# Kernel tuning notes

Hardware: AMD Instinct MI355X
Metric: run time of the kernel (lower is better)

## Reference

```python
import jax, jax.numpy as jnp
import numpy as np

R_ACT = 8
GROUPS = 32
EPS = 1e-5


def _group_norm(x, gamma, beta):
    # x: [B, C, T]; GroupNorm over (C//G, T) per group, per sample
    B, C, T = x.shape
    xr = x.reshape(B, GROUPS, C // GROUPS, T)
    mu = xr.mean(axis=(2, 3), keepdims=True)
    var = xr.var(axis=(2, 3), keepdims=True)
    xn = ((xr - mu) * jax.lax.rsqrt(var + EPS)).reshape(B, C, T)
    return xn * gamma[None, :, None] + beta[None, :, None]


def _topk_mean(logits, valid_len):
    # logits: [B, T, C]; valid_len: [B] int32. mean of top-k per class, k = max(1, valid_len // r_act)
    B, T, C = logits.shape
    vals = -jnp.sort(-logits, axis=1)            # descending sort along T
    csum = jnp.cumsum(vals, axis=1)              # [B, T, C]
    k = jnp.maximum(1, valid_len // R_ACT).astype(jnp.int32)  # [B]
    idx = jnp.broadcast_to((k - 1)[:, None, None], (B, 1, C))
    sel = jnp.take_along_axis(csum, idx, axis=1)[:, 0, :]     # [B, C]
    return sel / k[:, None].astype(logits.dtype)


def setup_inputs() -> dict:
    key = jax.random.key(0)
    ks = jax.random.split(key, 12)
    B, Fd, T, O, Timg, D, C = 16, 2048, 2048, 512, 2048, 512, 20
    inp = {
        "input_features": jax.random.normal(ks[0], (B, Fd, T), jnp.float32),
        "masks": jnp.ones((B, 1, T), jnp.float32),
        "text_proto": jax.random.normal(ks[1], (1, C, D), jnp.float32),
        "img_feats": jax.random.normal(ks[2], (B, Timg, D), jnp.float32),
        "img_masks": jnp.ones((B, Timg), jnp.float32),
        # 1x1-conv embedding params (2 layers) + GN affines + cls linear
        "W1": jax.random.normal(ks[3], (O, Fd), jnp.float32) * 0.02,
        "b1": jnp.zeros((O,), jnp.float32),
        "g1": jnp.ones((O,), jnp.float32),
        "beta1": jnp.zeros((O,), jnp.float32),
        "W2": jax.random.normal(ks[4], (O, O), jnp.float32) * 0.02,
        "b2": jnp.zeros((O,), jnp.float32),
        "g2": jnp.ones((O,), jnp.float32),
        "beta2": jnp.zeros((O,), jnp.float32),
        "Wc": jax.random.normal(ks[5], (C, O), jnp.float32) * 0.02,
        "bc": jnp.zeros((C,), jnp.float32),
    }
    return inp


def reference(input_features, masks, text_proto, img_feats, img_masks,
              W1, b1, g1, beta1, W2, b2, g2, beta2, Wc, bc):
    # feature embedding: two (1x1 conv -> GN) blocks, mask applied after each
    x = jnp.einsum('of,bft->bot', W1, input_features) + b1[None, :, None]
    x = _group_norm(x, g1, beta1) * masks
    x = jnp.einsum('oc,bct->bot', W2, x) + b2[None, :, None]
    x = _group_norm(x, g2, beta2) * masks            # [B, O, T]
    fe = x.transpose(0, 2, 1)                        # [B, T, O]
    cls_logits = jax.nn.sigmoid(jnp.einsum('bto,co->btc', fe, Wc) + bc)  # [B, T, C]

    tp = text_proto[0].T                             # [D, C]
    text_logits = jnp.einsum('btd,dc->btc', img_feats, tp)  # [B, Timg, C]

    text_len = jax.lax.stop_gradient(img_masks).sum(-1).astype(jnp.int32)      # [B]
    cls_len = jax.lax.stop_gradient(masks).sum(axis=(-2, -1)).astype(jnp.int32)  # [B]
    text_vid_scores = _topk_mean(text_logits, text_len)  # [B, C]
    cls_vid_scores = _topk_mean(cls_logits, cls_len)     # [B, C]
    # stack both heads: [0] = text (inference output), [1] = cls (training output)
    return jnp.stack([text_vid_scores, cls_vid_scores])
```

## Files before the change

### kernel.cpp

```cpp
#include <hip/hip_runtime.h>

typedef unsigned short u16;
typedef unsigned int u32;
typedef unsigned long long u64;

typedef __attribute__((ext_vector_type(8))) __bf16 bf16x8;
typedef __attribute__((ext_vector_type(4))) float f32x4;

__device__ __forceinline__ u16 f2bf(float f) {
  u32 u = __float_as_uint(f);
  u = (u + 0x7fffu + ((u >> 16) & 1u)) >> 16;
  return (u16)u;
}
__device__ __forceinline__ float bf2f(u16 h) {
  return __uint_as_float(((u32)h) << 16);
}

__device__ __forceinline__ void stage16(const u16* g, u16* lds_wave_base) {
#if __has_builtin(__builtin_amdgcn_global_load_lds)
  __builtin_amdgcn_global_load_lds((__attribute__((address_space(1))) u32*)g,
                                   (__attribute__((address_space(3))) u32*)lds_wave_base,
                                   16, 0, 0);
#else
  u16* l = lds_wave_base + (threadIdx.x & 63) * 8;
  *(uint4*)l = *(const uint4*)g;
#endif
}

__device__ __forceinline__ float wred(float v) {
  v += __shfl_xor(v, 1, 64);
  v += __shfl_xor(v, 2, 64);
  v += __shfl_xor(v, 4, 64);
  v += __shfl_xor(v, 8, 64);
  v += __shfl_xor(v, 16, 64);
  v += __shfl_xor(v, 32, 64);
  return v;
}

__global__ void __launch_bounds__(256) f2bf_kernel(const float* __restrict__ in,
                                                   u16* __restrict__ out, int n4) {
  int i = blockIdx.x * 256 + threadIdx.x;
  if (i >= n4) return;
  float4 v = ((const float4*)in)[i];
  u64 p = (u64)f2bf(v.x) | ((u64)f2bf(v.y) << 16) | ((u64)f2bf(v.z) << 32) |
          ((u64)f2bf(v.w) << 48);
  ((u64*)out)[i] = p;
}

__global__ void __launch_bounds__(256) zinit(float* __restrict__ p, int n) {
  int i = blockIdx.x * 256 + threadIdx.x;
  if (i < n) p[i] = 0.f;
}

__global__ void __launch_bounds__(256) transpose_bf16(const float* __restrict__ src,
                                                      u16* __restrict__ dst,
                                                      long long fStride, long long oStride) {
  __shared__ float tile[64][65];
  int b = blockIdx.z;
  const float* s = src + (size_t)b * fStride;
  u16* d = dst + (size_t)b * oStride;
  int tid = threadIdx.x;
  int t0 = blockIdx.x * 64, f0 = blockIdx.y * 64;
  int r = tid >> 2, cq = (tid & 3) * 16;
#pragma unroll
  for (int q = 0; q < 4; ++q) {
    float4 v = *(const float4*)(s + (size_t)(f0 + r) * 2048 + (t0 + cq + q * 4));
    tile[r][cq + q * 4 + 0] = v.x;
    tile[r][cq + q * 4 + 1] = v.y;
    tile[r][cq + q * 4 + 2] = v.z;
    tile[r][cq + q * 4 + 3] = v.w;
  }
  __syncthreads();
  u32 ow[8];
#pragma unroll
  for (int h = 0; h < 8; ++h) {
    float lo = tile[cq + 2 * h + 0][r];
    float hi = tile[cq + 2 * h + 1][r];
    ow[h] = (u32)f2bf(lo) | ((u32)f2bf(hi) << 16);
  }
  u16* dp = d + (size_t)(t0 + r) * 2048 + f0 + cq;
  uint4 v0 = {ow[0], ow[1], ow[2], ow[3]};
  uint4 v1 = {ow[4], ow[5], ow[6], ow[7]};
  *(uint4*)dp = v0;
  *(uint4*)(dp + 8) = v1;
}

#define BAR() __builtin_amdgcn_s_barrier()
#define LGKM0() asm volatile("s_waitcnt lgkmcnt(0)" ::: "memory")
#define VMC4() asm volatile("s_waitcnt vmcnt(4)" ::: "memory")
#define VMC0() asm volatile("s_waitcnt vmcnt(0)" ::: "memory")

__device__ __forceinline__ void rdA4(const u16 (&sAb)[256][32], int mh, int wm, int ln, int sl,
                                     bf16x8 (&af)[4]) {
#pragma unroll
  for (int mi = 0; mi < 4; ++mi)
    af[mi] = *(const bf16x8*)&sAb[wm * 128 + mh * 64 + mi * 16 + ln][sl];
}
__device__ __forceinline__ void rdB4(const u16 (&sBb)[256][32], int wn, int ln, int sl,
                                     bf16x8 (&bfr)[4]) {
#pragma unroll
  for (int ni = 0; ni < 4; ++ni)
    bfr[ni] = *(const bf16x8*)&sBb[wn * 64 + ni * 16 + ln][sl];
}
__device__ __forceinline__ void mfma8(f32x4 (&acc)[8][4], const bf16x8 (&af)[4],
                                      const bf16x8 (&bfr)[4], int mh) {
  __builtin_amdgcn_s_setprio(1);
#pragma unroll
  for (int mi = 0; mi < 4; ++mi)
#pragma unroll
    for (int ni = 0; ni < 4; ++ni)
      acc[mh * 4 + mi][ni] = __builtin_amdgcn_mfma_f32_16x16x32_bf16(
          af[mi], bfr[ni], acc[mh * 4 + mi][ni], 0, 0, 0);
  __builtin_amdgcn_s_setprio(0);
}
__device__ __forceinline__ void stg2(const u16* g0, const u16* g1, u16 (&dst)[256][32],
                                     int wid, int koff) {
  stage16(g0 + koff, &dst[wid * 32][0]);
  stage16(g1 + koff, &dst[wid * 32 + 16][0]);
}

template <bool MASKED>
__global__ void __launch_bounds__(512, 2) gemm8(const u16* __restrict__ A,
                                                const u16* __restrict__ A0,
                                                const u16* __restrict__ Bw,
                                                size_t bStride,
                                                const float* __restrict__ t1,
                                                const float* __restrict__ t2,
                                                const float* __restrict__ mkp,
                                                float* __restrict__ sOut,
                                                float* __restrict__ ssOut,
                                                u16* __restrict__ Out,
                                                int M, int N, int K) {
  __shared__ u16 sA[2][2][256][32];
  __shared__ u16 sB[2][2][256][32];
  int tid = threadIdx.x;
  int bz = blockIdx.z;
  int m0 = blockIdx.x * 256, n0 = blockIdx.y * 256;
  const u16* Ab = (bz == 0) ? A0 : (A + (size_t)bz * M * K);
  const u16* Bb = Bw + (size_t)bz * bStride;
  int lane = tid & 63, wid = tid >> 6;
  int wm = wid >> 2, wn = wid & 3;
  int ln = lane & 15, lm = lane >> 4;
  int sl = (lm ^ (ln & 3)) * 8;
  int lrow = lane >> 2;
  int swz = (lane & 3) ^ (lrow & 3);
  const u16* gA0 = Ab + (size_t)(m0 + wid * 32 + lrow) * K + swz * 8;
  const u16* gA1 = gA0 + (size_t)16 * K;
  const u16* gB0 = Bb + (size_t)(n0 + wid * 32 + lrow) * K + swz * 8;
  const u16* gB1 = gB0 + (size_t)16 * K;

  f32x4 acc[8][4];
#pragma unroll
  for (int mi = 0; mi < 8; ++mi)
#pragma unroll
    for (int ni = 0; ni < 4; ++ni) acc[mi][ni] = (f32x4){0.f, 0.f, 0.f, 0.f};

  bf16x8 af[4], bfr[4];

  stg2(gA0, gA1, sA[0][0], wid, 0);
  stg2(gB0, gB1, sB[0][0], wid, 0);
  stg2(gA0, gA1, sA[0][1], wid, 32);
  stg2(gB0, gB1, sB[0][1], wid, 32);
  stg2(gA0, gA1, sA[1][0], wid, 64);
  stg2(gB0, gB1, sB[1][0], wid, 64);
  VMC4();
  BAR();

  int NI = K >> 7;
  int kt0 = 0;
  for (int I = 0; I < NI - 1; ++I, kt0 += 2) {
    int kb1 = (kt0 + 1) * 64 + 32;
    int kb2 = (kt0 + 2) * 64;
    int kb3 = (kt0 + 2) * 64 + 32;
    int kb4 = (kt0 + 3) * 64;
    rdB4(sB[0][0], wn, ln, sl, bfr);
    rdA4(sA[0][0], 0, wm, ln, sl, af);
    stg2(gA0, gA1, sA[1][1], wid, kb1);
    BAR(); LGKM0(); mfma8(acc, af, bfr, 0); BAR();
    rdA4(sA[0][0], 1, wm, ln, sl, af);
    stg2(gB0, gB1, sB[1][1], wid, kb1);
    BAR(); LGKM0(); mfma8(acc, af, bfr, 1); BAR();
    rdB4(sB[0][1], wn, ln, sl, bfr);
    rdA4(sA[0][1], 0, wm, ln, sl, af);
    stg2(gA0, gA1, sA[0][0], wid, kb2);
    BAR(); LGKM0(); mfma8(acc, af, bfr, 0); BAR();
    rdA4(sA[0][1], 1, wm, ln, sl, af);
    stg2(gB0, gB1, sB[0][0], wid, kb2);
    BAR(); LGKM0(); mfma8(acc, af, bfr, 1);
    VMC4(); BAR();
    rdB4(sB[1][0], wn, ln, sl, bfr);
    rdA4(sA[1][0], 0, wm, ln, sl, af);
    stg2(gA0, gA1, sA[0][1], wid, kb3);
    BAR(); LGKM0(); mfma8(acc, af, bfr, 0); BAR();
    rdA4(sA[1][0], 1, wm, ln, sl, af);
    stg2(gB0, gB1, sB[0][1], wid, kb3);
    BAR(); LGKM0(); mfma8(acc, af, bfr, 1); BAR();
    rdB4(sB[1][1], wn, ln, sl, bfr);
    rdA4(sA[1][1], 0, wm, ln, sl, af);
    stg2(gA0, gA1, sA[1][0], wid, kb4);
    BAR(); LGKM0(); mfma8(acc, af, bfr, 0); BAR();
    rdA4(sA[1][1], 1, wm, ln, sl, af);
    stg2(gB0, gB1, sB[1][0], wid, kb4);
    BAR(); LGKM0(); mfma8(acc, af, bfr, 1);
    VMC4(); BAR();
  }
  {
    int kb1 = (kt0 + 1) * 64 + 32;
    rdB4(sB[0][0], wn, ln, sl, bfr);
    rdA4(sA[0][0], 0, wm, ln, sl, af);
    stg2(gA0, gA1, sA[1][1], wid, kb1);
    BAR(); LGKM0(); mfma8(acc, af, bfr, 0); BAR();
    rdA4(sA[0][0], 1, wm, ln, sl, af);
    stg2(gB0, gB1, sB[1][1], wid, kb1);
    BAR(); LGKM0(); mfma8(acc, af, bfr, 1); BAR();
    rdB4(sB[0][1], wn, ln, sl, bfr);
    rdA4(sA[0][1], 0, wm, ln, sl, af);
    BAR(); LGKM0(); mfma8(acc, af, bfr, 0); BAR();
    rdA4(sA[0][1], 1, wm, ln, sl, af);
    BAR(); LGKM0(); mfma8(acc, af, bfr, 1);
    VMC0(); BAR();
    rdB4(sB[1][0], wn, ln, sl, bfr);
    rdA4(sA[1][0], 0, wm, ln, sl, af);
    BAR(); LGKM0(); mfma8(acc, af, bfr, 0); BAR();
    rdA4(sA[1][0], 1, wm, ln, sl, af);
    BAR(); LGKM0(); mfma8(acc, af, bfr, 1); BAR();
    rdB4(sB[1][1], wn, ln, sl, bfr);
    rdA4(sA[1][1], 0, wm, ln, sl, af);
    BAR(); LGKM0(); mfma8(acc, af, bfr, 0); BAR();
    rdA4(sA[1][1], 1, wm, ln, sl, af);
    LGKM0(); mfma8(acc, af, bfr, 1);
  }

  const float* t1p = MASKED ? (t1 + (size_t)bz * N) : t1;
  float t1v[4], t2v[4];
#pragma unroll
  for (int ni = 0; ni < 4; ++ni) {
    int ncol = n0 + wn * 64 + ni * 16 + ln;
    t1v[ni] = t1p[ncol];
    t2v[ni] = MASKED ? t2[ncol] : 0.f;
  }
  float sp[4] = {0.f, 0.f, 0.f, 0.f}, ssp[4] = {0.f, 0.f, 0.f, 0.f};
  u16* ob = Out + (size_t)bz * M * N;
#pragma unroll
  for (int mi = 0; mi < 8; ++mi) {
    int mrow = m0 + wm * 128 + mi * 16 + lm * 4;
    float mka[4] = {1.f, 1.f, 1.f, 1.f};
    if constexpr (MASKED) {
      float4 mv = *(const float4*)(mkp + (size_t)bz * M + mrow);
      mka[0] = mv.x; mka[1] = mv.y; mka[2] = mv.z; mka[3] = mv.w;
    }
#pragma unroll
    for (int ni = 0; ni < 4; ++ni) {
      int ncol = n0 + wn * 64 + ni * 16 + ln;
#pragma unroll
      for (int r = 0; r < 4; ++r) {
        float v = acc[mi][ni][r] + t1v[ni];
        if constexpr (MASKED) v = v * mka[r] + t2v[ni];
        sp[ni] += v;
        ssp[ni] += v * v;
        ob[(size_t)(mrow + r) * N + ncol] = f2bf(v);
      }
    }
  }
#pragma unroll
  for (int ni = 0; ni < 4; ++ni) {
    float S = wred(sp[ni]);
    float SS = wred(ssp[ni]);
    if (lane == 0) {
      int grp = blockIdx.y * 16 + wn * 4 + ni;
      atomicAdd(&sOut[bz * 32 + grp], S);
      atomicAdd(&ssOut[bz * 32 + grp], SS);
    }
  }
}

__global__ void __launch_bounds__(512) gnstats(const float* __restrict__ sS,
                                               const float* __restrict__ sSS,
                                               const float* __restrict__ gamma,
                                               const float* __restrict__ beta,
                                               float* __restrict__ gmO,
                                               float* __restrict__ gdO) {
  int b = blockIdx.x;
  int c = threadIdx.x;
  int g = c >> 4;
  const float cnt = 16.f * 2048.f;
  float mu = sS[b * 32 + g] / cnt;
  float var = sSS[b * 32 + g] / cnt - mu * mu;
  float inv = rsqrtf(var + 1e-5f);
  float gm = gamma[c] * inv;
  gmO[(size_t)b * 512 + c] = gm;
  gdO[(size_t)b * 512 + c] = beta[c] - mu * gm;
}

__global__ void __launch_bounds__(256) wfold(const float* __restrict__ W2,
                                             const float* __restrict__ gm1,
                                             const float* __restrict__ bt1,
                                             u16* __restrict__ W2f,
                                             float* __restrict__ beta2) {
  int w = blockIdx.x * 4 + (threadIdx.x >> 6);
  int lane = threadIdx.x & 63;
  int b = w >> 9, o = w & 511;
  const float* wr = W2 + (size_t)o * 512 + lane * 8;
  const float* gmr = gm1 + (size_t)b * 512 + lane * 8;
  const float* btr = bt1 + (size_t)b * 512 + lane * 8;
  float4 w0 = *(const float4*)wr, w1 = *(const float4*)(wr + 4);
  float4 g0 = *(const float4*)gmr, g1v = *(const float4*)(gmr + 4);
  float4 t0 = *(const float4*)btr, t1v = *(const float4*)(btr + 4);
  float wv[8] = {w0.x, w0.y, w0.z, w0.w, w1.x, w1.y, w1.z, w1.w};
  float gv[8] = {g0.x, g0.y, g0.z, g0.w, g1v.x, g1v.y, g1v.z, g1v.w};
  float tv[8] = {t0.x, t0.y, t0.z, t0.w, t1v.x, t1v.y, t1v.z, t1v.w};
  u32 ow[4];
  float acc = 0.f;
#pragma unroll
  for (int h = 0; h < 4; ++h) {
    float lo = wv[2 * h] * gv[2 * h];
    float hi = wv[2 * h + 1] * gv[2 * h + 1];
    ow[h] = (u32)f2bf(lo) | ((u32)f2bf(hi) << 16);
    acc += wv[2 * h] * tv[2 * h] + wv[2 * h + 1] * tv[2 * h + 1];
  }
  uint4 o4 = {ow[0], ow[1], ow[2], ow[3]};
  *(uint4*)(W2f + ((size_t)b * 512 + o) * 512 + lane * 8) = o4;
  acc = wred(acc);
  if (lane == 0) beta2[(size_t)b * 512 + o] = acc;
}

template <typename TX, bool CLS>
__global__ void __launch_bounds__(512) head_v2(const TX* __restrict__ X,
                                               const float* __restrict__ W,
                                               const float* __restrict__ bcv,
                                               const float* __restrict__ gma,
                                               const float* __restrict__ gad,
                                               const float* __restrict__ masks,
                                               float* __restrict__ Out, int Tdim) {
  __shared__ float red[64 * 20];
  int tid = threadIdx.x;
  int tl = tid & 63;
  int ks = __builtin_amdgcn_readfirstlane(tid >> 6);
  int b = blockIdx.y;
  int t = blockIdx.x * 64 + tl;
  for (int i = tid; i < 64 * 20; i += 512) red[i] = 0.f;
  float acc[20];
#pragma unroll
  for (int c = 0; c < 20; ++c) acc[c] = 0.f;
  const TX* xr = X + ((size_t)b * Tdim + t) * 512 + ks * 64;
  const float* Wk = W + ks * 64;
  const float* gmk = CLS ? (gma + (size_t)b * 512 + ks * 64) : nullptr;
  const float* gak = CLS ? (gad + (size_t)b * 512 + ks * 64) : nullptr;
  __syncthreads();
#pragma unroll
  for (int kk = 0; kk < 64; kk += 8) {
    float xv[8];
    if constexpr (sizeof(TX) == 2) {
      uint4 v = *(const uint4*)(xr + kk);
      u32 wv[4] = {v.x, v.y, v.z, v.w};
#pragma unroll
      for (int h = 0; h < 4; ++h) {
        xv[2 * h] = bf2f((u16)(wv[h] & 0xffffu));
        xv[2 * h + 1] = bf2f((u16)(wv[h] >> 16));
      }
    } else {
      float4 p0 = *(const float4*)(xr + kk);
      float4 p1 = *(const float4*)(xr + kk + 4);
      xv[0] = p0.x; xv[1] = p0.y; xv[2] = p0.z; xv[3] = p0.w;
      xv[4] = p1.x; xv[5] = p1.y; xv[6] = p1.z; xv[7] = p1.w;
    }
    if constexpr (CLS) {
#pragma unroll
      for (int j = 0; j < 8; ++j) xv[j] = xv[j] * gmk[kk + j] + gak[kk + j];
    }
#pragma unroll
    for (int c = 0; c < 20; ++c) {
      const float* wr = &Wk[c * 512 + kk];
#pragma unroll
      for (int j = 0; j < 8; ++j) acc[c] += xv[j] * wr[j];
    }
  }
#pragma unroll
  for (int c = 0; c < 20; ++c) atomicAdd(&red[tl * 20 + c], acc[c]);
  __syncthreads();
  if (tid < 64) {
    float mk = CLS ? masks[(size_t)b * Tdim + t] : 1.f;
#pragma unroll
    for (int c = 0; c < 20; ++c) {
      float v = red[tid * 20 + c];
      if constexpr (CLS) {
        v = v * mk + bcv[c];
        v = 1.f / (1.f + __expf(-v));
      }
      Out[((size_t)b * 20 + c) * Tdim + t] = v;
    }
  }
}

__global__ void __launch_bounds__(256) topk_sel(const float* __restrict__ textL,
                                                const float* __restrict__ clsL,
                                                const float* __restrict__ img_masks,
                                                const float* __restrict__ masks,
                                                float* __restrict__ out) {
  __shared__ u32 keys[2048];
  __shared__ u32 hist[256];
  __shared__ u32 sel[2];
  __shared__ float rbuf[4], rbuf2[4];
  int bx = blockIdx.x;
  int head = bx / 320, rem = bx - head * 320;
  int b = rem / 20, c = rem - b * 20;
  int tid = threadIdx.x;
  const float* mk = head ? (masks + (size_t)b * 2048) : (img_masks + (size_t)b * 2048);
  float ls = 0.f;
  for (int i = tid; i < 2048; i += 256) ls += mk[i];
  ls = wred(ls);
  if ((tid & 63) == 0) rbuf[tid >> 6] = ls;
  const float* rowp = (head ? clsL : textL) + ((size_t)(b * 20 + c)) * 2048;
  for (int i = tid; i < 2048; i += 256) {
    u32 u = __float_as_uint(rowp[i]);
    u32 sgn = (u32)((int)u >> 31);
    keys[i] = u ^ (sgn | 0x80000000u);
  }
  __syncthreads();
  int len = (int)(rbuf[0] + rbuf[1] + rbuf[2] + rbuf[3]);
  u32 k = (u32)(len >> 3);
  if (k < 1) k = 1;
  u32 want = k, prefix = 0;
#pragma unroll
  for (int byt = 3; byt >= 0; --byt) {
    int sh = byt * 8;
    hist[tid] = 0;
    __syncthreads();
    for (int i = tid; i < 2048; i += 256) {
      u32 kk = keys[i];
      bool match = (byt == 3) || ((kk >> (sh + 8)) == (prefix >> (sh + 8)));
      if (match) atomicAdd(&hist[(kk >> sh) & 0xffu], 1u);
    }
    __syncthreads();
    if (tid < 64) {
      int r0 = tid * 4;
      u32 h0 = hist[255 - r0], h1 = hist[254 - r0], h2 = hist[253 - r0], h3 = hist[252 - r0];
      u32 p0 = h0, p1 = p0 + h1, p2 = p1 + h2, p3 = p2 + h3;
      u32 inc = p3;
#pragma unroll
      for (int off = 1; off < 64; off <<= 1) {
        u32 t = __shfl_up(inc, off, 64);
        if (tid >= off) inc += t;
      }
      u32 excl = inc - p3;
      u32 S0 = excl + p0, S1 = excl + p1, S2 = excl + p2, S3 = excl + p3;
      if (S0 >= want && excl < want) { sel[0] = (u32)(255 - r0); sel[1] = want - excl; }
      if (S1 >= want && S0 < want)   { sel[0] = (u32)(254 - r0); sel[1] = want - S0; }
      if (S2 >= want && S1 < want)   { sel[0] = (u32)(253 - r0); sel[1] = want - S1; }
      if (S3 >= want && S2 < want)   { sel[0] = (u32)(252 - r0); sel[1] = want - S2; }
    }
    __syncthreads();
    prefix |= sel[0] << sh;
    want = sel[1];
    __syncthreads();
  }
  float s = 0.f, cg = 0.f;
  for (int i = tid; i < 2048; i += 256) {
    u32 kk = keys[i];
    if (kk > prefix) {
      u32 u = (kk & 0x80000000u) ? (kk ^ 0x80000000u) : ~kk;
      s += __uint_as_float(u);
      cg += 1.f;
    }
  }
  s = wred(s);
  cg = wred(cg);
  if ((tid & 63) == 0) { rbuf[tid >> 6] = s; rbuf2[tid >> 6] = cg; }
  __syncthreads();
  if (tid == 0) {
    float S = rbuf[0] + rbuf[1] + rbuf[2] + rbuf[3];
    float CG = rbuf2[0] + rbuf2[1] + rbuf2[2] + rbuf2[3];
    u32 u = (prefix & 0x80000000u) ? (prefix ^ 0x80000000u) : ~prefix;
    float thr = __uint_as_float(u);
    S += ((float)k - CG) * thr;
    out[bx] = S / (float)k;
  }
}

extern "C" void kernel_launch(void* const* d_in, const int* in_sizes, int n_in,
                              void* d_out, int out_size, void* d_ws, size_t ws_size,
                              hipStream_t stream) {
  const float* F          = (const float*)d_in[0];
  const float* masks      = (const float*)d_in[1];
  const float* text_proto = (const float*)d_in[2];
  const float* img_feats  = (const float*)d_in[3];
  const float* img_masks  = (const float*)d_in[4];
  const float* W1 = (const float*)d_in[5];
  const float* b1 = (const float*)d_in[6];
  const float* g1 = (const float*)d_in[7];
  const float* be1 = (const float*)d_in[8];
  const float* W2 = (const float*)d_in[9];
  const float* b2 = (const float*)d_in[10];
  const float* g2 = (const float*)d_in[11];
  const float* be2 = (const float*)d_in[12];
  const float* Wc = (const float*)d_in[13];
  const float* bc = (const float*)d_in[14];
  float* out = (float*)d_out;

  const int T = 2048, Fd = 2048, O = 512;
  char* w = (char*)d_ws;
  u16* W1b     = (u16*)(w);
  u16* x1      = (u16*)(w + 2621440);
  float* clsL  = (float*)(w + 36175872);
  float* textL = (float*)(w + 38797312);
  float* gma   = (float*)(w + 41418752);
  float* gad   = (float*)(w + 41451520);
  const size_t oEnd0 = 41484288;
  const size_t ftBytes = (size_t)16 * T * Fd * 2;
  const size_t EXTRA = 8388608 + 3 * 32768 + 8192;

  bool bigws = ws_size >= oEnd0 + ftBytes + EXTRA;
  char* ext = bigws ? (w + oEnd0 + ftBytes)
                    : (w + oEnd0 + (size_t)T * Fd * 2 + (size_t)16 * T * O * 2);
  u16* W2f    = (u16*)ext;
  float* gm1  = (float*)(ext + 8388608);
  float* bt1  = gm1 + 16 * 512;
  float* beta2 = bt1 + 16 * 512;
  float* sbase = beta2 + 16 * 512;
  float* s1 = sbase, *ss1 = sbase + 512, *s2 = sbase + 1024, *ss2 = sbase + 1536;

  f2bf_kernel<<<1024, 256, 0, stream>>>(W1, W1b, (O * Fd) / 4);
  zinit<<<8, 256, 0, stream>>>(sbase, 2048);

  const u16 *FtA, *FtA0;
  u16* x2;
  if (bigws) {
    u16* Ft = (u16*)(w + oEnd0);
    transpose_bf16<<<dim3(32, 32, 16), 256, 0, stream>>>(F, Ft, (long long)Fd * T,
                                                         (long long)T * Fd);
    FtA = Ft; FtA0 = Ft; x2 = Ft;
  } else {
    u16* ft0 = (u16*)(w + oEnd0);
    x2 = (u16*)(w + oEnd0 + (size_t)T * Fd * 2);
    for (int b = 0; b < 16; ++b) {
      u16* dst = (b == 0) ? ft0 : ((u16*)d_in[0]) + (size_t)b * T * Fd;
      transpose_bf16<<<dim3(32, 32, 1), 256, 0, stream>>>(F + (size_t)b * Fd * T, dst, 0, 0);
    }
    FtA = (const u16*)d_in[0]; FtA0 = ft0;
  }

  gemm8<false><<<dim3(8, 2, 16), 512, 0, stream>>>(FtA, FtA0, W1b, 0, b1, nullptr, nullptr,
                                                   s1, ss1, x1, 2048, 512, 2048);
  gnstats<<<16, 512, 0, stream>>>(s1, ss1, g1, be1, gm1, bt1);
  wfold<<<2048, 256, 0, stream>>>(W2, gm1, bt1, W2f, beta2);
  gemm8<true><<<dim3(8, 2, 16), 512, 0, stream>>>(x1, x1, W2f, (size_t)512 * 512, beta2, b2,
                                                  masks, s2, ss2, x2, 2048, 512, 512);
  gnstats<<<16, 512, 0, stream>>>(s2, ss2, g2, be2, gma, gad);
  head_v2<u16, true><<<dim3(32, 16), 512, 0, stream>>>(x2, Wc, bc, gma, gad, masks, clsL, 2048);
  head_v2<float, false><<<dim3(32, 16), 512, 0, stream>>>(img_feats, text_proto, nullptr,
                                                          nullptr, nullptr, nullptr, textL, 2048);
  topk_sel<<<640, 256, 0, stream>>>(textL, clsL, img_masks, masks, out);
}
```

Before: 664.4 us.

## Fuse prep, GN-stats, weight-fold and head kernels to cut launches

Merges the W1 bf16 conversion and stats zeroing into the transpose launch as an extra z-slice. Folds GroupNorm statistics computation into the W2-fold kernel and into a combined heads kernel. That combined kernel handles both the cls and text heads in one launch and replaces LDS atomics with a per-wave buffer plus a reduction. The goal is fewer kernel launches and less serialization overhead; the cost is some stats math repeated in every block.

```diff
diff --git a/kernel.cpp b/kernel.cpp
--- a/kernel.cpp
+++ b/kernel.cpp
@@ -59,6 +59,54 @@
   int b = blockIdx.z;
   const float* s = src + (size_t)b * fStride;
   u16* d = dst + (size_t)b * oStride;
+  int tid = threadIdx.x;
+  int t0 = blockIdx.x * 64, f0 = blockIdx.y * 64;
+  int r = tid >> 2, cq = (tid & 3) * 16;
+#pragma unroll
+  for (int q = 0; q < 4; ++q) {
+    float4 v = *(const float4*)(s + (size_t)(f0 + r) * 2048 + (t0 + cq + q * 4));
+    tile[r][cq + q * 4 + 0] = v.x;
+    tile[r][cq + q * 4 + 1] = v.y;
+    tile[r][cq + q * 4 + 2] = v.z;
+    tile[r][cq + q * 4 + 3] = v.w;
+  }
+  __syncthreads();
+  u32 ow[8];
+#pragma unroll
+  for (int h = 0; h < 8; ++h) {
+    float lo = tile[cq + 2 * h + 0][r];
+    float hi = tile[cq + 2 * h + 1][r];
+    ow[h] = (u32)f2bf(lo) | ((u32)f2bf(hi) << 16);
+  }
+  u16* dp = d + (size_t)(t0 + r) * 2048 + f0 + cq;
+  uint4 v0 = {ow[0], ow[1], ow[2], ow[3]};
+  uint4 v1 = {ow[4], ow[5], ow[6], ow[7]};
+  *(uint4*)dp = v0;
+  *(uint4*)(dp + 8) = v1;
+}
+
+__global__ void __launch_bounds__(256) prep_kernel(const float* __restrict__ F,
+                                                   u16* __restrict__ Ft,
+                                                   const float* __restrict__ W1,
+                                                   u16* __restrict__ W1b,
+                                                   float* __restrict__ sbase) {
+  if (blockIdx.z == 16) {
+    int bid = blockIdx.y * 32 + blockIdx.x;
+    int tid = threadIdx.x;
+    if (bid == 0) {
+      for (int q = tid; q < 2048; q += 256) sbase[q] = 0.f;
+    }
+    int i = bid * 256 + tid;
+    float4 v = ((const float4*)W1)[i];
+    u64 p = (u64)f2bf(v.x) | ((u64)f2bf(v.y) << 16) | ((u64)f2bf(v.z) << 32) |
+            ((u64)f2bf(v.w) << 48);
+    ((u64*)W1b)[i] = p;
+    return;
+  }
+  __shared__ float tile[64][65];
+  int b = blockIdx.z;
+  const float* s = F + (size_t)b * 2048 * 2048;
+  u16* d = Ft + (size_t)b * 2048 * 2048;
   int tid = threadIdx.x;
   int t0 = blockIdx.x * 64, f0 = blockIdx.y * 64;
   int r = tid >> 2, cq = (tid & 3) * 16;
@@ -274,83 +322,94 @@
   }
 }
 
-__global__ void __launch_bounds__(512) gnstats(const float* __restrict__ sS,
-                                               const float* __restrict__ sSS,
-                                               const float* __restrict__ gamma,
-                                               const float* __restrict__ beta,
-                                               float* __restrict__ gmO,
-                                               float* __restrict__ gdO) {
-  int b = blockIdx.x;
-  int c = threadIdx.x;
-  int g = c >> 4;
-  const float cnt = 16.f * 2048.f;
-  float mu = sS[b * 32 + g] / cnt;
-  float var = sSS[b * 32 + g] / cnt - mu * mu;
-  float inv = rsqrtf(var + 1e-5f);
-  float gm = gamma[c] * inv;
-  gmO[(size_t)b * 512 + c] = gm;
-  gdO[(size_t)b * 512 + c] = beta[c] - mu * gm;
-}
-
-__global__ void __launch_bounds__(256) wfold(const float* __restrict__ W2,
-                                             const float* __restrict__ gm1,
-                                             const float* __restrict__ bt1,
-                                             u16* __restrict__ W2f,
-                                             float* __restrict__ beta2) {
+__global__ void __launch_bounds__(256) wfold2(const float* __restrict__ W2,
+                                              const float* __restrict__ s1,
+                                              const float* __restrict__ ss1,
+                                              const float* __restrict__ g1,
+                                              const float* __restrict__ be1,
+                                              u16* __restrict__ W2f,
+                                              float* __restrict__ beta2) {
   int w = blockIdx.x * 4 + (threadIdx.x >> 6);
   int lane = threadIdx.x & 63;
   int b = w >> 9, o = w & 511;
-  const float* wr = W2 + (size_t)o * 512 + lane * 8;
-  const float* gmr = gm1 + (size_t)b * 512 + lane * 8;
-  const float* btr = bt1 + (size_t)b * 512 + lane * 8;
+  int c0 = lane * 8;
+  int g = c0 >> 4;
+  const float cnt = 16.f * 2048.f;
+  float mu = s1[b * 32 + g] / cnt;
+  float var = ss1[b * 32 + g] / cnt - mu * mu;
+  float inv = rsqrtf(var + 1e-5f);
+  const float* wr = W2 + (size_t)o * 512 + c0;
+  const float* gr = g1 + c0;
+  const float* br = be1 + c0;
   float4 w0 = *(const float4*)wr, w1 = *(const float4*)(wr + 4);
-  float4 g0 = *(const float4*)gmr, g1v = *(const float4*)(gmr + 4);
-  float4 t0 = *(const float4*)btr, t1v = *(const float4*)(btr + 4);
+  float4 q0 = *(const float4*)gr, q1 = *(const float4*)(gr + 4);
+  float4 p0 = *(const float4*)br, p1 = *(const float4*)(br + 4);
   float wv[8] = {w0.x, w0.y, w0.z, w0.w, w1.x, w1.y, w1.z, w1.w};
-  float gv[8] = {g0.x, g0.y, g0.z, g0.w, g1v.x, g1v.y, g1v.z, g1v.w};
-  float tv[8] = {t0.x, t0.y, t0.z, t0.w, t1v.x, t1v.y, t1v.z, t1v.w};
+  float gmv[8], btv[8];
+  float qv[8] = {q0.x, q0.y, q0.z, q0.w, q1.x, q1.y, q1.z, q1.w};
+  float pv[8] = {p0.x, p0.y, p0.z, p0.w, p1.x, p1.y, p1.z, p1.w};
+#pragma unroll
+  for (int j = 0; j < 8; ++j) {
+    gmv[j] = qv[j] * inv;
+    btv[j] = pv[j] - mu * gmv[j];
+  }
   u32 ow[4];
   float acc = 0.f;
 #pragma unroll
   for (int h = 0; h < 4; ++h) {
-    float lo = wv[2 * h] * gv[2 * h];
-    float hi = wv[2 * h + 1] * gv[2 * h + 1];
+    float lo = wv[2 * h] * gmv[2 * h];
+    float hi = wv[2 * h + 1] * gmv[2 * h + 1];
     ow[h] = (u32)f2bf(lo) | ((u32)f2bf(hi) << 16);
-    acc += wv[2 * h] * tv[2 * h] + wv[2 * h + 1] * tv[2 * h + 1];
+    acc += wv[2 * h] * btv[2 * h] + wv[2 * h + 1] * btv[2 * h + 1];
   }
   uint4 o4 = {ow[0], ow[1], ow[2], ow[3]};
-  *(uint4*)(W2f + ((size_t)b * 512 + o) * 512 + lane * 8) = o4;
+  *(uint4*)(W2f + ((size_t)b * 512 + o) * 512 + c0) = o4;
   acc = wred(acc);
   if (lane == 0) beta2[(size_t)b * 512 + o] = acc;
 }
 
-template <typename TX, bool CLS>
-__global__ void __launch_bounds__(512) head_v2(const TX* __restrict__ X,
-                                               const float* __restrict__ W,
-                                               const float* __restrict__ bcv,
-                                               const float* __restrict__ gma,
-                                               const float* __restrict__ gad,
-                                               const float* __restrict__ masks,
-                                               float* __restrict__ Out, int Tdim) {
-  __shared__ float red[64 * 20];
+__global__ void __launch_bounds__(512) heads_all(const u16* __restrict__ X2,
+                                                 const float* __restrict__ Wc,
+                                                 const float* __restrict__ bcv,
+                                                 const float* __restrict__ s2,
+                                                 const float* __restrict__ ss2,
+                                                 const float* __restrict__ g2,
+                                                 const float* __restrict__ be2,
+                                                 const float* __restrict__ masks,
+                                                 const float* __restrict__ imgF,
+                                                 const float* __restrict__ tproto,
+                                                 float* __restrict__ clsL,
+                                                 float* __restrict__ textL) {
+  __shared__ float red[8][64][20];
+  __shared__ float gmS[512], gdS[512];
   int tid = threadIdx.x;
   int tl = tid & 63;
   int ks = __builtin_amdgcn_readfirstlane(tid >> 6);
+  int w = tid >> 6;
   int b = blockIdx.y;
   int t = blockIdx.x * 64 + tl;
-  for (int i = tid; i < 64 * 20; i += 512) red[i] = 0.f;
+  bool cls = (blockIdx.z == 0);
+  if (cls) {
+    int c = tid;
+    int g = c >> 4;
+    const float cnt = 16.f * 2048.f;
+    float mu = s2[b * 32 + g] / cnt;
+    float var = ss2[b * 32 + g] / cnt - mu * mu;
+    float inv = rsqrtf(var + 1e-5f);
+    float gm = g2[c] * inv;
+    gmS[c] = gm;
+    gdS[c] = be2[c] - mu * gm;
+  }
+  __syncthreads();
   float acc[20];
 #pragma unroll
   for (int c = 0; c < 20; ++c) acc[c] = 0.f;
-  const TX* xr = X + ((size_t)b * Tdim + t) * 512 + ks * 64;
-  const float* Wk = W + ks * 64;
-  const float* gmk = CLS ? (gma + (size_t)b * 512 + ks * 64) : nullptr;
-  const float* gak = CLS ? (gad + (size_t)b * 512 + ks * 64) : nullptr;
-  __syncthreads();
-#pragma unroll
-  for (int kk = 0; kk < 64; kk += 8) {
-    float xv[8];
-    if constexpr (sizeof(TX) == 2) {
+  if (cls) {
+    const u16* xr = X2 + ((size_t)b * 2048 + t) * 512 + ks * 64;
+    const float* Wk = Wc + ks * 64;
+#pragma unroll
+    for (int kk = 0; kk < 64; kk += 8) {
+      float xv[8];
       uint4 v = *(const uint4*)(xr + kk);
       u32 wv[4] = {v.x, v.y, v.z, v.w};
 #pragma unroll
@@ -358,36 +417,54 @@
         xv[2 * h] = bf2f((u16)(wv[h] & 0xffffu));
         xv[2 * h + 1] = bf2f((u16)(wv[h] >> 16));
       }
-    } else {
+#pragma unroll
+      for (int j = 0; j < 8; ++j)
+        xv[j] = xv[j] * gmS[ks * 64 + kk + j] + gdS[ks * 64 + kk + j];
+#pragma unroll
+      for (int c = 0; c < 20; ++c) {
+        const float* wr = &Wk[c * 512 + kk];
+#pragma unroll
+        for (int j = 0; j < 8; ++j) acc[c] += xv[j] * wr[j];
+      }
+    }
+  } else {
+    const float* xr = imgF + ((size_t)b * 2048 + t) * 512 + ks * 64;
+    const float* Wk = tproto + ks * 64;
+#pragma unroll
+    for (int kk = 0; kk < 64; kk += 8) {
+      float xv[8];
       float4 p0 = *(const float4*)(xr + kk);
       float4 p1 = *(const float4*)(xr + kk + 4);
       xv[0] = p0.x; xv[1] = p0.y; xv[2] = p0.z; xv[3] = p0.w;
       xv[4] = p1.x; xv[5] = p1.y; xv[6] = p1.z; xv[7] = p1.w;
-    }
-    if constexpr (CLS) {
-#pragma unroll
-      for (int j = 0; j < 8; ++j) xv[j] = xv[j] * gmk[kk + j] + gak[kk + j];
-    }
-#pragma unroll
-    for (int c = 0; c < 20; ++c) {
-      const float* wr = &Wk[c * 512 + kk];
-#pragma unroll
-      for (int j = 0; j < 8; ++j) acc[c] += xv[j] * wr[j];
-    }
-  }
-#pragma unroll
-  for (int c = 0; c < 20; ++c) atomicAdd(&red[tl * 20 + c], acc[c]);
+#pragma unroll
+      for (int c = 0; c < 20; ++c) {
+        const float* wr = &Wk[c * 512 + kk];
+#pragma unroll
+        for (int j = 0; j < 8; ++j) acc[c] += xv[j] * wr[j];
+      }
+    }
+  }
+#pragma unroll
+  for (int c4 = 0; c4 < 5; ++c4) {
+    float4 v = {acc[c4 * 4 + 0], acc[c4 * 4 + 1], acc[c4 * 4 + 2], acc[c4 * 4 + 3]};
+    *(float4*)&red[w][tl][c4 * 4] = v;
+  }
   __syncthreads();
-  if (tid < 64) {
-    float mk = CLS ? masks[(size_t)b * Tdim + t] : 1.f;
-#pragma unroll
-    for (int c = 0; c < 20; ++c) {
-      float v = red[tid * 20 + c];
-      if constexpr (CLS) {
-        v = v * mk + bcv[c];
-        v = 1.f / (1.f + __expf(-v));
-      }
-      Out[((size_t)b * 20 + c) * Tdim + t] = v;
+  for (int idx = tid; idx < 1280; idx += 512) {
+    int tl2 = idx / 20;
+    int c = idx - tl2 * 20;
+    float v = 0.f;
+#pragma unroll
+    for (int w2 = 0; w2 < 8; ++w2) v += red[w2][tl2][c];
+    int t2 = blockIdx.x * 64 + tl2;
+    if (cls) {
+      float mk = masks[(size_t)b * 2048 + t2];
+      v = v * mk + bcv[c];
+      v = 1.f / (1.f + __expf(-v));
+      clsL[((size_t)(b * 20 + c)) * 2048 + t2] = v;
+    } else {
+      textL[((size_t)(b * 20 + c)) * 2048 + t2] = v;
     }
   }
 }
@@ -503,33 +580,27 @@
   u16* x1      = (u16*)(w + 2621440);
   float* clsL  = (float*)(w + 36175872);
   float* textL = (float*)(w + 38797312);
-  float* gma   = (float*)(w + 41418752);
-  float* gad   = (float*)(w + 41451520);
   const size_t oEnd0 = 41484288;
   const size_t ftBytes = (size_t)16 * T * Fd * 2;
-  const size_t EXTRA = 8388608 + 3 * 32768 + 8192;
+  const size_t EXTRA = 8388608 + 32768 + 8192;
 
   bool bigws = ws_size >= oEnd0 + ftBytes + EXTRA;
   char* ext = bigws ? (w + oEnd0 + ftBytes)
                     : (w + oEnd0 + (size_t)T * Fd * 2 + (size_t)16 * T * O * 2);
-  u16* W2f    = (u16*)ext;
-  float* gm1  = (float*)(ext + 8388608);
-  float* bt1  = gm1 + 16 * 512;
-  float* beta2 = bt1 + 16 * 512;
+  u16* W2f     = (u16*)ext;
+  float* beta2 = (float*)(ext + 8388608);
   float* sbase = beta2 + 16 * 512;
   float* s1 = sbase, *ss1 = sbase + 512, *s2 = sbase + 1024, *ss2 = sbase + 1536;
-
-  f2bf_kernel<<<1024, 256, 0, stream>>>(W1, W1b, (O * Fd) / 4);
-  zinit<<<8, 256, 0, stream>>>(sbase, 2048);
 
   const u16 *FtA, *FtA0;
   u16* x2;
   if (bigws) {
     u16* Ft = (u16*)(w + oEnd0);
-    transpose_bf16<<<dim3(32, 32, 16), 256, 0, stream>>>(F, Ft, (long long)Fd * T,
-                                                         (long long)T * Fd);
+    prep_kernel<<<dim3(32, 32, 17), 256, 0, stream>>>(F, Ft, W1, W1b, sbase);
     FtA = Ft; FtA0 = Ft; x2 = Ft;
   } else {
+    f2bf_kernel<<<1024, 256, 0, stream>>>(W1, W1b, (O * Fd) / 4);
+    zinit<<<8, 256, 0, stream>>>(sbase, 2048);
     u16* ft0 = (u16*)(w + oEnd0);
     x2 = (u16*)(w + oEnd0 + (size_t)T * Fd * 2);
     for (int b = 0; b < 16; ++b) {
@@ -541,13 +612,10 @@
 
   gemm8<false><<<dim3(8, 2, 16), 512, 0, stream>>>(FtA, FtA0, W1b, 0, b1, nullptr, nullptr,
                                                    s1, ss1, x1, 2048, 512, 2048);
-  gnstats<<<16, 512, 0, stream>>>(s1, ss1, g1, be1, gm1, bt1);
-  wfold<<<2048, 256, 0, stream>>>(W2, gm1, bt1, W2f, beta2);
+  wfold2<<<2048, 256, 0, stream>>>(W2, s1, ss1, g1, be1, W2f, beta2);
   gemm8<true><<<dim3(8, 2, 16), 512, 0, stream>>>(x1, x1, W2f, (size_t)512 * 512, beta2, b2,
                                                   masks, s2, ss2, x2, 2048, 512, 512);
-  gnstats<<<16, 512, 0, stream>>>(s2, ss2, g2, be2, gma, gad);
-  head_v2<u16, true><<<dim3(32, 16), 512, 0, stream>>>(x2, Wc, bc, gma, gad, masks, clsL, 2048);
-  head_v2<float, false><<<dim3(32, 16), 512, 0, stream>>>(img_feats, text_proto, nullptr,
-                                                          nullptr, nullptr, nullptr, textL, 2048);
+  heads_all<<<dim3(32, 16, 2), 512, 0, stream>>>(x2, Wc, bc, s2, ss2, g2, be2, masks,
+                                                 img_feats, text_proto, clsL, textL);
   topk_sel<<<640, 256, 0, stream>>>(textL, clsL, img_masks, masks, out);
 }
```

After: 618.6 us. 1.07x faster.
